# Kernel optimization log

Measured on AMD Instinct MI355X. Metric: run time of the kernel, lower is better.

## Reference

```python
import jax, jax.numpy as jnp
import numpy as np

B, S, D, NH, A, K, N_ITER = 512, 200, 512, 8, 512, 2, 3
DK = D // NH
L = 2 * K  # max local window length
NEG = -1e9


def make_pe_table(d, max_len):
    pos = np.arange(max_len)[:, None].astype(np.float64)
    j = np.arange(d)[None, :]
    ang = pos / np.power(10000.0, 2.0 * (j // 2) / d)
    pe = np.zeros((max_len, d))
    pe[:, 0::2] = np.sin(ang[:, 0::2])
    pe[:, 1::2] = np.cos(ang[:, 1::2])
    pe = np.concatenate([np.zeros((1, d)), pe], axis=0)  # pad row at index 0
    return jnp.asarray(pe, jnp.float32)


def layer_norm(x, g, b, eps=1e-5):
    m = jnp.mean(x, axis=-1, keepdims=True)
    v = jnp.mean((x - m) ** 2, axis=-1, keepdims=True)
    return (x - m) / jnp.sqrt(v + eps) * g + b


def setup_inputs() -> dict:
    key = jax.random.key(0)
    ks = jax.random.split(key, 24)
    p = lambda k, shape, s=0.02: jax.random.normal(k, shape, jnp.float32) * s
    embedded = jax.random.normal(ks[0], (B, S, D), jnp.float32)
    stc_lens = jax.random.randint(ks[1], (B,), 8, S + 1, jnp.int32)
    offsets = jnp.minimum(jax.random.randint(ks[2], (B,), 0, S, jnp.int32), stc_lens - 1)
    sep_lst = jnp.sort(jax.random.randint(ks[3], (B, 2), 0, S, jnp.int32), axis=1)
    return dict(
        embedded=embedded, stc_lens=stc_lens, offsets=offsets, sep_lst=sep_lst,
        W1=p(ks[4], (D, A)), W2=p(ks[5], (A, 1)),
        ln_g=jnp.ones((D,), jnp.float32), ln_b=jnp.zeros((D,), jnp.float32),
        lng_g=jnp.ones((D,), jnp.float32), lng_b=jnp.zeros((D,), jnp.float32),
        Wq=p(ks[6], (D, D)), bq=jnp.zeros((D,), jnp.float32),
        Wk=p(ks[7], (D, D)), bk=jnp.zeros((D,), jnp.float32),
        Wv=p(ks[8], (D, D)), bv=jnp.zeros((D,), jnp.float32),
        W_ih=p(ks[9], (3 * D, D)), W_hh=p(ks[10], (3 * D, D)),
        b_ih=jnp.zeros((3 * D,), jnp.float32), b_hh=jnp.zeros((3 * D,), jnp.float32),
        seg_emb=p(ks[11], (2, D)),
        pe_table=make_pe_table(D, S),
    )


def _forward(embedded, W1, W2, ln_g, ln_b, lng_g, lng_b, Wq, bq, Wk, bk, Wv, bv,
             W_ih, W_hh, b_ih, b_hh, seg_emb, pe_table, stc_lens, offsets, sep_lst):
    nsep = sep_lst.shape[1]
    bidx = jnp.arange(B)
    # ---- LocalVisiblePooling: per-sample window [start, end) around offset ----
    idx = jnp.sum(sep_lst < offsets[:, None], axis=1)  # segment index containing pos
    prev_sep = sep_lst[bidx, jnp.clip(idx - 1, 0, nsep - 1)]
    left = jnp.where(idx > 0, prev_sep + 1, 0)
    next_sep = sep_lst[bidx, jnp.clip(idx, 0, nsep - 1)]
    right = jnp.where(idx < nsep, next_sep, stc_lens)
    start = jnp.maximum(offsets - K, left)
    end = jnp.minimum(offsets + K, right)
    inds = start[:, None] + jnp.arange(L)  # [B, L]
    valid = inds < end[:, None]
    ic = jnp.clip(inds, 0, S - 1)
    h_blk = embedded[bidx[:, None], ic] * valid[..., None].astype(embedded.dtype)  # [B,L,D]
    a = jnp.tanh(h_blk @ W1) @ W2  # [B, L, 1]
    s1 = jax.nn.softmax(a[..., 0], axis=0)  # faithful to Softmax(dim=1) over batch dim
    score = jax.nn.softmax(jnp.where(valid, s1, NEG), axis=1)  # masked softmax over window
    b0_bf = jnp.einsum('bl,bld->bd', score, h_blk)  # [B, D]
    # ---- relative positional encoding for H ----
    x = jnp.arange(S)[None, :]  # [1, S]
    pos = offsets[:, None]
    ip = jnp.where(x < pos, pos - x, x + 1 - pos)
    ip = jnp.where(x < stc_lens[:, None], ip, 0)
    ip = jnp.clip(ip, 0, S)
    seg = (x >= pos).astype(jnp.int32)
    H = embedded + pe_table[ip] + seg_emb[seg]  # [B, S, D]
    H = layer_norm(H, ln_g, ln_b)
    b_t = layer_norm(b0_bf + pe_table[0], ln_g, ln_b)  # 'b' pe is the zero pad row
    # ---- GlobalUpdate: sigmoid-attention MHA (q_len=1) + GRUCell, N iterations ----
    pad = x >= stc_lens[:, None]  # [B, S] True where padded
    kproj = (H @ Wk + bk).reshape(B, S, NH, DK)
    vproj = (H @ Wv + bv).reshape(B, S, NH, DK)
    scale = 1.0 / jnp.sqrt(jnp.float32(DK))
    for _ in range(N_ITER):
        q = (b_t @ Wq + bq).reshape(B, NH, DK)
        scores = jnp.einsum('bhd,bshd->bhs', q, kproj) * scale
        scores = jnp.where(pad[:, None, :], NEG, scores)
        p_attn = jax.nn.sigmoid(scores)  # non-standard sigmoid attention
        m_t = jnp.einsum('bhs,bshd->bhd', p_attn, vproj).reshape(B, D)
        m_t = layer_norm(m_t, lng_g, lng_b)
        gi = m_t @ W_ih.T + b_ih
        gh = b_t @ W_hh.T + b_hh
        ir, iz, inn = jnp.split(gi, 3, axis=-1)
        hr, hz, hn = jnp.split(gh, 3, axis=-1)
        r = jax.nn.sigmoid(ir + hr)
        z = jax.nn.sigmoid(iz + hz)
        n = jnp.tanh(inn + r * hn)
        b_t = (1.0 - z) * n + z * b_t
    return b_t[:, None, :]  # [B, 1, D]


def reference(embedded, stc_lens, offsets, sep_lst, W1, W2, ln_g, ln_b, lng_g, lng_b,
              Wq, bq, Wk, bk, Wv, bv, W_ih, W_hh, b_ih, b_hh, seg_emb, pe_table):
    return _forward(embedded, W1, W2, ln_g, ln_b, lng_g, lng_b, Wq, bq, Wk, bk, Wv, bv,
                    W_ih, W_hh, b_ih, b_hh, seg_emb, pe_table, stc_lens, offsets, sep_lst)
```

## Files before the change

### kernel.cpp

```cpp
#include <hip/hip_runtime.h>
#include <hip/hip_bf16.h>
#include <math.h>

constexpr int B_   = 512;
constexpr int S_   = 200;
constexpr int D_   = 512;
constexpr int NH_  = 8;
constexpr int DK_  = 64;
constexpr int LBLK = 4;
constexpr int NITER = 3;
constexpr int TD_  = 1536;
#define NEGV (-1000000000.0f)

using bf16 = __hip_bfloat16;
typedef __attribute__((ext_vector_type(8))) short bf16x8;
typedef __attribute__((ext_vector_type(4))) float f32x4;

__device__ __forceinline__ float wred(float x) {
#pragma unroll
    for (int o = 32; o; o >>= 1) x += __shfl_xor(x, o);
    return x;
}

__global__ void __launch_bounds__(256) k_cvt(const float* __restrict__ src,
                                             bf16* __restrict__ dst, int n) {
    int i = blockIdx.x * 256 + threadIdx.x;
    if (i < n) dst[i] = __float2bfloat16(src[i]);
}

__global__ void __launch_bounds__(256) k_tcvt(const float* __restrict__ src,
                                              bf16* __restrict__ dst) {
    int i = blockIdx.x * 256 + threadIdx.x;
    if (i >= D_ * TD_) return;
    int k = i / TD_, n = i - k * TD_;
    dst[i] = __float2bfloat16(src[n * D_ + k]);
}

__global__ void __launch_bounds__(256) k_blockscore(
        const float* __restrict__ emb, const float* __restrict__ W1,
        const float* __restrict__ W2, const int* __restrict__ stc,
        const int* __restrict__ offs, const int* __restrict__ sep,
        float* __restrict__ hblk, float* __restrict__ a_out,
        int* __restrict__ se_out) {
    int b = blockIdx.x;
    int t = threadIdx.x;
    int off = offs[b], slen = stc[b];
    int sA = sep[b * 2 + 0], sB = sep[b * 2 + 1];
    int idx = (sA < off ? 1 : 0) + (sB < off ? 1 : 0);
    int prev = (idx == 2) ? sB : sA;
    int nxt  = (idx == 0) ? sA : sB;
    int left = (idx > 0) ? prev + 1 : 0;
    int right = (idx < 2) ? nxt : slen;
    int start = max(off - 2, left);
    int end   = min(off + 2, right);

    __shared__ float hs[LBLK][D_];
    {
        int l = t >> 6, lane = t & 63;
        int ind = start + l;
        bool valid = ind < end;
        float v0x=0,v0y=0,v0z=0,v0w=0,v1x=0,v1y=0,v1z=0,v1w=0;
        if (valid) {
            int ic = min(max(ind, 0), S_ - 1);
            const float* src = emb + ((size_t)b * S_ + ic) * D_ + lane * 8;
            float4 u0 = *(const float4*)src;
            float4 u1 = *(const float4*)(src + 4);
            v0x=u0.x; v0y=u0.y; v0z=u0.z; v0w=u0.w;
            v1x=u1.x; v1y=u1.y; v1z=u1.z; v1w=u1.w;
        }
        int base = lane * 8;
        hs[l][base+0]=v0x; hs[l][base+1]=v0y; hs[l][base+2]=v0z; hs[l][base+3]=v0w;
        hs[l][base+4]=v1x; hs[l][base+5]=v1y; hs[l][base+6]=v1z; hs[l][base+7]=v1w;
        float* g = hblk + ((size_t)b * LBLK + l) * D_ + base;
        g[0]=v0x; g[1]=v0y; g[2]=v0z; g[3]=v0w; g[4]=v1x; g[5]=v1y; g[6]=v1z; g[7]=v1w;
    }
    __syncthreads();

    float pa0 = 0.f, pa1 = 0.f, pa2 = 0.f, pa3 = 0.f;
#pragma unroll
    for (int cc = 0; cc < 2; ++cc) {
        int col = t + cc * 256;
        float a0 = 0.f, a1 = 0.f, a2 = 0.f, a3 = 0.f;
        for (int d = 0; d < D_; ++d) {
            float w = W1[(size_t)d * 512 + col];
            a0 += hs[0][d] * w; a1 += hs[1][d] * w;
            a2 += hs[2][d] * w; a3 += hs[3][d] * w;
        }
        float w2 = W2[col];
        pa0 += tanhf(a0) * w2; pa1 += tanhf(a1) * w2;
        pa2 += tanhf(a2) * w2; pa3 += tanhf(a3) * w2;
    }
    __shared__ float red[256];
    float pv[4] = {pa0, pa1, pa2, pa3};
#pragma unroll
    for (int l = 0; l < 4; ++l) {
        red[t] = pv[l]; __syncthreads();
        for (int st = 128; st; st >>= 1) {
            if (t < st) red[t] += red[t + st];
            __syncthreads();
        }
        if (t == 0) a_out[b * 4 + l] = red[0];
        __syncthreads();
    }
    if (t == 0) { se_out[b * 2] = start; se_out[b * 2 + 1] = end; }
}

__global__ void __launch_bounds__(512) k_score(const float* __restrict__ a_in,
                                               const int* __restrict__ se,
                                               float* __restrict__ score) {
    int b = threadIdx.x;
    float av[4], s1[4];
#pragma unroll
    for (int l = 0; l < 4; ++l) av[l] = a_in[b * 4 + l];
    __shared__ float red[512];
#pragma unroll
    for (int l = 0; l < 4; ++l) {
        red[b] = av[l]; __syncthreads();
        for (int st = 256; st; st >>= 1) {
            if (b < st) red[b] = fmaxf(red[b], red[b + st]);
            __syncthreads();
        }
        float mx = red[0]; __syncthreads();
        float e = expf(av[l] - mx);
        red[b] = e; __syncthreads();
        for (int st = 256; st; st >>= 1) {
            if (b < st) red[b] += red[b + st];
            __syncthreads();
        }
        s1[l] = e / red[0];
        __syncthreads();
    }
    int start = se[b * 2], end = se[b * 2 + 1];
    float x[4], mx2 = -1e30f;
#pragma unroll
    for (int l = 0; l < 4; ++l) {
        x[l] = (start + l < end) ? s1[l] : NEGV;
        mx2 = fmaxf(mx2, x[l]);
    }
    float s = 0.f, e4[4];
#pragma unroll
    for (int l = 0; l < 4; ++l) { e4[l] = expf(x[l] - mx2); s += e4[l]; }
    float inv = 1.f / s;
#pragma unroll
    for (int l = 0; l < 4; ++l) score[b * 4 + l] = e4[l] * inv;
}

__global__ void __launch_bounds__(64) k_b0(
        const float* __restrict__ hblk, const float* __restrict__ score,
        const float* __restrict__ pe, const float* __restrict__ g,
        const float* __restrict__ bb, float* __restrict__ bt,
        bf16* __restrict__ btb) {
    int b = blockIdx.x, lane = threadIdx.x;
    float sc0 = score[b*4+0], sc1 = score[b*4+1], sc2 = score[b*4+2], sc3 = score[b*4+3];
    const float* hb = hblk + (size_t)b * LBLK * D_ + lane * 8;
    float v[8];
#pragma unroll
    for (int j = 0; j < 8; ++j) {
        float x = pe[lane * 8 + j];
        x += sc0 * hb[j] + sc1 * hb[D_ + j] + sc2 * hb[2*D_ + j] + sc3 * hb[3*D_ + j];
        v[j] = x;
    }
    float sum = 0.f;
#pragma unroll
    for (int j = 0; j < 8; ++j) sum += v[j];
    sum = wred(sum);
    float mean = sum * (1.f / 512.f);
    float sq = 0.f;
#pragma unroll
    for (int j = 0; j < 8; ++j) { float c = v[j] - mean; sq += c * c; }
    sq = wred(sq);
    float rstd = rsqrtf(sq * (1.f / 512.f) + 1e-5f);
#pragma unroll
    for (int j = 0; j < 8; ++j) {
        int d = lane * 8 + j;
        float y = (v[j] - mean) * rstd * g[d] + bb[d];
        bt[(size_t)b * D_ + d] = y;
        btb[(size_t)b * D_ + d] = __float2bfloat16(y);
    }
}

__global__ void __launch_bounds__(256) k_H(
        const float* __restrict__ emb, const float* __restrict__ pe,
        const float* __restrict__ seg_emb, const float* __restrict__ g,
        const float* __restrict__ bb, const int* __restrict__ stc,
        const int* __restrict__ offs, bf16* __restrict__ Hc,
        int b0, int nrows) {
    int rid = blockIdx.x * 4 + (threadIdx.x >> 6);
    if (rid >= nrows) return;
    int lane = threadIdx.x & 63;
    int bl = rid / S_;
    int s = rid - bl * S_;
    int b = b0 + bl;
    int slen = stc[b];
    if (s >= slen) return;
    int pos = offs[b];
    int ip = (s < pos) ? (pos - s) : (s + 1 - pos);
    if (ip > S_) ip = S_;
    int seg = (s >= pos) ? 1 : 0;
    const float* er = emb + ((size_t)b * S_ + s) * D_ + lane * 8;
    const float* pr = pe + (size_t)ip * D_ + lane * 8;
    const float* sr = seg_emb + seg * D_ + lane * 8;
    float4 e0 = *(const float4*)er, e1 = *(const float4*)(er + 4);
    float4 p0 = *(const float4*)pr, p1 = *(const float4*)(pr + 4);
    float4 q0 = *(const float4*)sr, q1 = *(const float4*)(sr + 4);
    float v[8];
    v[0]=e0.x+p0.x+q0.x; v[1]=e0.y+p0.y+q0.y; v[2]=e0.z+p0.z+q0.z; v[3]=e0.w+p0.w+q0.w;
    v[4]=e1.x+p1.x+q1.x; v[5]=e1.y+p1.y+q1.y; v[6]=e1.z+p1.z+q1.z; v[7]=e1.w+p1.w+q1.w;
    float sum = 0.f;
#pragma unroll
    for (int j = 0; j < 8; ++j) sum += v[j];
    sum = wred(sum);
    float mean = sum * (1.f / 512.f);
    float sq = 0.f;
#pragma unroll
    for (int j = 0; j < 8; ++j) { float c = v[j] - mean; sq += c * c; }
    sq = wred(sq);
    float rstd = rsqrtf(sq * (1.f / 512.f) + 1e-5f);
    union { uint4 u; bf16 h[8]; } o;
#pragma unroll
    for (int j = 0; j < 8; ++j) {
        int d = lane * 8 + j;
        o.h[j] = __float2bfloat16((v[j] - mean) * rstd * g[d] + bb[d]);
    }
    *(uint4*)(Hc + ((size_t)bl * S_ + s) * D_ + lane * 8) = o.u;
}

__device__ __forceinline__ void gemm_tile64(
        const bf16* __restrict__ Abase, int lda,
        const bf16* __restrict__ Bbase, int ldb,
        const float* __restrict__ bias,
        float* __restrict__ Cf, bf16* __restrict__ Cb, int ldc,
        int rows_valid) {
    __shared__ bf16 As[64][40];
    __shared__ bf16 BsT[64][40];
    int t = threadIdx.x;
    int lane = t & 63, w = t >> 6;
    f32x4 acc0 = {0.f,0.f,0.f,0.f}, acc1 = {0.f,0.f,0.f,0.f};
    f32x4 acc2 = {0.f,0.f,0.f,0.f}, acc3 = {0.f,0.f,0.f,0.f};
    int arow = t >> 2, ac8 = (t & 3) * 8;
    int bn = t & 63, bkb = (t >> 6) * 8;

    for (int k0 = 0; k0 < 512; k0 += 32) {
        *(uint4*)&As[arow][ac8] =
            *(const uint4*)(Abase + (size_t)arow * lda + k0 + ac8);
        {
            union { uint4 u; bf16 h[8]; } tmp;
#pragma unroll
            for (int j = 0; j < 8; ++j)
                tmp.h[j] = Bbase[(size_t)(k0 + bkb + j) * ldb + bn];
            *(uint4*)&BsT[bn][bkb] = tmp.u;
        }
        __syncthreads();
        bf16x8 bfrag = *(const bf16x8*)&BsT[w * 16 + (lane & 15)][(lane >> 4) * 8];
        bf16x8 a0 = *(const bf16x8*)&As[ 0 + (lane & 15)][(lane >> 4) * 8];
        bf16x8 a1 = *(const bf16x8*)&As[16 + (lane & 15)][(lane >> 4) * 8];
        bf16x8 a2 = *(const bf16x8*)&As[32 + (lane & 15)][(lane >> 4) * 8];
        bf16x8 a3 = *(const bf16x8*)&As[48 + (lane & 15)][(lane >> 4) * 8];
        acc0 = __builtin_amdgcn_mfma_f32_16x16x32_bf16(a0, bfrag, acc0, 0, 0, 0);
        acc1 = __builtin_amdgcn_mfma_f32_16x16x32_bf16(a1, bfrag, acc1, 0, 0, 0);
        acc2 = __builtin_amdgcn_mfma_f32_16x16x32_bf16(a2, bfrag, acc2, 0, 0, 0);
        acc3 = __builtin_amdgcn_mfma_f32_16x16x32_bf16(a3, bfrag, acc3, 0, 0, 0);
        __syncthreads();
    }
    int col = w * 16 + (lane & 15);
    float bvv = bias[col];
    int rbase = (lane >> 4) * 4;
    f32x4 av[4] = {acc0, acc1, acc2, acc3};
#pragma unroll
    for (int rb = 0; rb < 4; ++rb) {
#pragma unroll
        for (int r = 0; r < 4; ++r) {
            int row = rb * 16 + rbase + r;
            if (row < rows_valid) {
                float vv = av[rb][r] + bvv;
                if (Cf) Cf[(size_t)row * ldc + col] = vv;
                if (Cb) Cb[(size_t)row * ldc + col] = __float2bfloat16(vv);
            }
        }
    }
}

__global__ void __launch_bounds__(256) k_gemm_kv(
        const bf16* __restrict__ Hc, const bf16* __restrict__ Wk,
        const bf16* __restrict__ Wv, const float* __restrict__ bk,
        const float* __restrict__ bv, bf16* __restrict__ kvk,
        bf16* __restrict__ kvv, const int* __restrict__ stc, int b0) {
    int nt = blockIdx.x;
    int s0 = blockIdx.y * 64;
    int bl = blockIdx.z;
    int b = b0 + bl;
    int slen = stc[b];
    if (s0 >= slen) return;
    const bf16* A = Hc + ((size_t)bl * S_ + s0) * D_;
    const bf16* Bm; bf16* C; const float* bias; int n0;
    if (nt < 8) { Bm = Wk; C = kvk; bias = bk; n0 = nt * 64; }
    else        { Bm = Wv; C = kvv; bias = bv; n0 = (nt - 8) * 64; }
    int rows_valid = min(64, slen - s0);
    gemm_tile64(A, D_, Bm + n0, D_, bias + n0,
                nullptr, C + ((size_t)b * S_ + s0) * D_ + n0, D_, rows_valid);
}

__global__ void __launch_bounds__(256) k_gemm_flat(
        const bf16* __restrict__ A, int lda, const bf16* __restrict__ Bm, int ldb,
        const float* __restrict__ bias, float* __restrict__ Cf,
        bf16* __restrict__ Cb, int ldc) {
    int n0 = blockIdx.x * 64, m0 = blockIdx.y * 64;
    gemm_tile64(A + (size_t)m0 * lda, lda, Bm + n0, ldb, bias + n0,
                Cf ? Cf + (size_t)m0 * ldc + n0 : nullptr,
                Cb ? Cb + (size_t)m0 * ldc + n0 : nullptr, ldc, 64);
}

__global__ void __launch_bounds__(256) k_attn(
        const float* __restrict__ q, const bf16* __restrict__ kk,
        const bf16* __restrict__ vv, const int* __restrict__ stc,
        const float* __restrict__ lng_g, const float* __restrict__ lng_b,
        float* __restrict__ mf, bf16* __restrict__ mb) {
    int b = blockIdx.x;
    int t = threadIdx.x, w = t >> 6, lane = t & 63;
    int slen = stc[b];
    const float* qp = q + (size_t)b * D_ + lane * 8;
    float4 qa = *(const float4*)qp, qb4 = *(const float4*)(qp + 4);
    float qv[8] = {qa.x, qa.y, qa.z, qa.w, qb4.x, qb4.y, qb4.z, qb4.w};
    float acc[8] = {0,0,0,0,0,0,0,0};
    const bf16* kbase = kk + (size_t)b * S_ * D_ + lane * 8;
    const bf16* vbase = vv + (size_t)b * S_ * D_ + lane * 8;
    for (int s = w; s < slen; s += 4) {
        union { uint4 u; bf16 h[8]; } kl, vl;
        kl.u = *(const uint4*)(kbase + (size_t)s * D_);
        float part = 0.f;
#pragma unroll
        for (int j = 0; j < 8; ++j) part += qv[j] * __bfloat162float(kl.h[j]);
        part += __shfl_xor(part, 1);
        part += __shfl_xor(part, 2);
        part += __shfl_xor(part, 4);
        float p = 1.f / (1.f + __expf(-part * 0.125f));
        vl.u = *(const uint4*)(vbase + (size_t)s * D_);
#pragma unroll
        for (int j = 0; j < 8; ++j) acc[j] += p * __bfloat162float(vl.h[j]);
    }
    __shared__ float macc[4][D_];
#pragma unroll
    for (int j = 0; j < 8; ++j) macc[w][lane * 8 + j] = acc[j];
    __syncthreads();
    __shared__ float red[256];
    int d1 = t + 256;
    float x0 = macc[0][t] + macc[1][t] + macc[2][t] + macc[3][t];
    float x1 = macc[0][d1] + macc[1][d1] + macc[2][d1] + macc[3][d1];
    red[t] = x0 + x1; __syncthreads();
    for (int st = 128; st; st >>= 1) {
        if (t < st) red[t] += red[t + st];
        __syncthreads();
    }
    float mean = red[0] * (1.f / 512.f); __syncthreads();
    float c0 = x0 - mean, c1 = x1 - mean;
    red[t] = c0 * c0 + c1 * c1; __syncthreads();
    for (int st = 128; st; st >>= 1) {
        if (t < st) red[t] += red[t + st];
        __syncthreads();
    }
    float rstd = rsqrtf(red[0] * (1.f / 512.f) + 1e-5f);
    float y0 = c0 * rstd * lng_g[t] + lng_b[t];
    float y1 = c1 * rstd * lng_g[d1] + lng_b[d1];
    mf[(size_t)b * D_ + t] = y0;
    mf[(size_t)b * D_ + d1] = y1;
    mb[(size_t)b * D_ + t] = __float2bfloat16(y0);
    mb[(size_t)b * D_ + d1] = __float2bfloat16(y1);
}

__global__ void __launch_bounds__(256) k_gru(
        const float* __restrict__ gi, const float* __restrict__ gh,
        float* __restrict__ bt, bf16* __restrict__ btb) {
    int i = blockIdx.x * 256 + threadIdx.x;
    int b = i >> 9, d = i & 511;
    const float* gib = gi + (size_t)b * TD_;
    const float* ghb = gh + (size_t)b * TD_;
    float ir = gib[d], iz = gib[512 + d], inn = gib[1024 + d];
    float hr = ghb[d], hz = ghb[512 + d], hn = ghb[1024 + d];
    float r = 1.f / (1.f + expf(-(ir + hr)));
    float z = 1.f / (1.f + expf(-(iz + hz)));
    float n = tanhf(inn + r * hn);
    float bo = bt[i];
    float bn = (1.f - z) * n + z * bo;
    bt[i] = bn;
    btb[i] = __float2bfloat16(bn);
}

extern "C" void kernel_launch(void* const* d_in, const int* in_sizes, int n_in,
                              void* d_out, int out_size, void* d_ws, size_t ws_size,
                              hipStream_t stream) {
    const float* emb   = (const float*)d_in[0];
    const int*   stc   = (const int*)d_in[1];
    const int*   offs  = (const int*)d_in[2];
    const int*   sep   = (const int*)d_in[3];
    const float* W1    = (const float*)d_in[4];
    const float* W2    = (const float*)d_in[5];
    const float* ln_g  = (const float*)d_in[6];
    const float* ln_b  = (const float*)d_in[7];
    const float* lng_g = (const float*)d_in[8];
    const float* lng_b = (const float*)d_in[9];
    const float* Wq    = (const float*)d_in[10];
    const float* bq    = (const float*)d_in[11];
    const float* Wk    = (const float*)d_in[12];
    const float* bk    = (const float*)d_in[13];
    const float* Wv    = (const float*)d_in[14];
    const float* bv    = (const float*)d_in[15];
    const float* W_ih  = (const float*)d_in[16];
    const float* W_hh  = (const float*)d_in[17];
    const float* b_ih  = (const float*)d_in[18];
    const float* b_hh  = (const float*)d_in[19];
    const float* seg_e = (const float*)d_in[20];
    const float* pe    = (const float*)d_in[21];

    char* base = (char*)d_ws;
    size_t off = 0;
    auto alloc = [&](size_t bytes) -> void* {
        off = (off + 255) & ~(size_t)255;
        void* r = base + off;
        off += bytes;
        return r;
    };
    bf16* kvk = (bf16*)alloc((size_t)(B_ * S_ + 64) * D_ * 2);
    bf16* kvv = (bf16*)alloc((size_t)(B_ * S_ + 64) * D_ * 2);
    float* hblk = (float*)alloc((size_t)B_ * LBLK * D_ * 4);
    float* a_s  = (float*)alloc((size_t)B_ * 4 * 4);
    float* scr  = (float*)alloc((size_t)B_ * 4 * 4);
    int*   se   = (int*)alloc((size_t)B_ * 2 * 4);
    float* bt   = (float*)alloc((size_t)B_ * D_ * 4);
    bf16*  btb  = (bf16*)alloc((size_t)B_ * D_ * 2);
    float* qb   = (float*)alloc((size_t)B_ * D_ * 4);
    float* mf   = (float*)alloc((size_t)B_ * D_ * 4);
    bf16*  mb   = (bf16*)alloc((size_t)B_ * D_ * 2);
    float* gi   = (float*)alloc((size_t)B_ * TD_ * 4);
    float* gh   = (float*)alloc((size_t)B_ * TD_ * 4);
    bf16* Wq_b  = (bf16*)alloc((size_t)D_ * D_ * 2);
    bf16* Wk_b  = (bf16*)alloc((size_t)D_ * D_ * 2);
    bf16* Wv_b  = (bf16*)alloc((size_t)D_ * D_ * 2);
    bf16* WihT  = (bf16*)alloc((size_t)D_ * TD_ * 2);
    bf16* WhhT  = (bf16*)alloc((size_t)D_ * TD_ * 2);

    auto hbytes = [](int ch) { return ((size_t)ch * S_ + 64) * D_ * 2; };
    int CH = 512;
    {
        size_t used = (off + 255) & ~(size_t)255;
        size_t remain = (ws_size > used) ? (ws_size - used) : 0;
        if (hbytes(512) + 256 > remain) CH = 64;
        if (CH == 64 && hbytes(64) + 256 > remain) CH = 16;
    }
    bf16* Hc = (bf16*)alloc(hbytes(CH));

    k_cvt<<<(D_ * D_ + 255) / 256, 256, 0, stream>>>(Wq, Wq_b, D_ * D_);
    k_cvt<<<(D_ * D_ + 255) / 256, 256, 0, stream>>>(Wk, Wk_b, D_ * D_);
    k_cvt<<<(D_ * D_ + 255) / 256, 256, 0, stream>>>(Wv, Wv_b, D_ * D_);
    k_tcvt<<<(D_ * TD_ + 255) / 256, 256, 0, stream>>>(W_ih, WihT);
    k_tcvt<<<(D_ * TD_ + 255) / 256, 256, 0, stream>>>(W_hh, WhhT);

    k_blockscore<<<B_, 256, 0, stream>>>(emb, W1, W2, stc, offs, sep, hblk, a_s, se);
    k_score<<<1, 512, 0, stream>>>(a_s, se, scr);
    k_b0<<<B_, 64, 0, stream>>>(hblk, scr, pe, ln_g, ln_b, bt, btb);

    for (int c = 0; c < B_; c += CH) {
        int rows = CH * S_;
        k_H<<<(rows + 3) / 4, 256, 0, stream>>>(emb, pe, seg_e, ln_g, ln_b,
                                                stc, offs, Hc, c, rows);
        k_gemm_kv<<<dim3(16, 4, CH), 256, 0, stream>>>(Hc, Wk_b, Wv_b, bk, bv,
                                                       kvk, kvv, stc, c);
    }

    for (int it = 0; it < NITER; ++it) {
        k_gemm_flat<<<dim3(8, 8), 256, 0, stream>>>(btb, D_, Wq_b, D_, bq,
                                                    qb, nullptr, D_);
        k_attn<<<B_, 256, 0, stream>>>(qb, kvk, kvv, stc, lng_g, lng_b, mf, mb);
        k_gemm_flat<<<dim3(24, 8), 256, 0, stream>>>(mb, D_, WihT, TD_, b_ih,
                                                     gi, nullptr, TD_);
        k_gemm_flat<<<dim3(24, 8), 256, 0, stream>>>(btb, D_, WhhT, TD_, b_hh,
                                                     gh, nullptr, TD_);
        k_gru<<<(B_ * D_) / 256, 256, 0, stream>>>(gi, gh, bt, btb);
    }
    hipMemcpyAsync(d_out, bt, (size_t)out_size * sizeof(float),
                   hipMemcpyDeviceToDevice, stream);
}
```

Before: 844.2 us.

## Rework GEMMs with N-major weights, LDS direct loads, fused K/V and gate launches

Weights are pre-transposed to N-by-K bf16 layout so both GEMM operands can be loaded into LDS with direct global-to-LDS 16-byte loads, replacing the strided scalar B gathers. A templated GEMM core supports larger tiles, and K and V projections are fused into one 64x256-tiled GEMM writing an interleaved KV buffer. The two GRU gate GEMMs now share one launch, and the weight conversions are merged into a single prep kernel. The interleaved KV layout changes attention's memory stride, and the larger tiles reduce the number of blocks.

```diff
diff --git a/kernel.cpp b/kernel.cpp
--- a/kernel.cpp
+++ b/kernel.cpp
@@ -5,8 +5,6 @@
 constexpr int B_   = 512;
 constexpr int S_   = 200;
 constexpr int D_   = 512;
-constexpr int NH_  = 8;
-constexpr int DK_  = 64;
 constexpr int LBLK = 4;
 constexpr int NITER = 3;
 constexpr int TD_  = 1536;
@@ -22,18 +20,38 @@
     return x;
 }
 
-__global__ void __launch_bounds__(256) k_cvt(const float* __restrict__ src,
-                                             bf16* __restrict__ dst, int n) {
+__device__ __forceinline__ void gload16(const bf16* g, bf16* l) {
+    __builtin_amdgcn_global_load_lds(
+        (const __attribute__((address_space(1))) void*)g,
+        (__attribute__((address_space(3))) void*)l, 16, 0, 0);
+}
+
+__global__ void __launch_bounds__(256) k_prep(
+        const float* __restrict__ Wq, const float* __restrict__ Wk,
+        const float* __restrict__ Wv, const float* __restrict__ bk,
+        const float* __restrict__ bv, const float* __restrict__ Wih,
+        const float* __restrict__ Whh, bf16* __restrict__ WqT,
+        bf16* __restrict__ WkvT, float* __restrict__ bkv,
+        bf16* __restrict__ Wih_b, bf16* __restrict__ Whh_b) {
     int i = blockIdx.x * 256 + threadIdx.x;
-    if (i < n) dst[i] = __float2bfloat16(src[i]);
-}
-
-__global__ void __launch_bounds__(256) k_tcvt(const float* __restrict__ src,
-                                              bf16* __restrict__ dst) {
-    int i = blockIdx.x * 256 + threadIdx.x;
-    if (i >= D_ * TD_) return;
-    int k = i / TD_, n = i - k * TD_;
-    dst[i] = __float2bfloat16(src[n * D_ + k]);
+    if (i < 512 * 512) {
+        int n = i >> 9, k = i & 511;
+        WqT[i] = __float2bfloat16(Wq[k * 512 + n]);
+        return;
+    }
+    i -= 512 * 512;
+    if (i < 1024 * 512) {
+        int n = i >> 9, k = i & 511;
+        WkvT[i] = __float2bfloat16(n < 512 ? Wk[k * 512 + n]
+                                           : Wv[k * 512 + (n - 512)]);
+        return;
+    }
+    i -= 1024 * 512;
+    if (i < TD_ * D_) { Wih_b[i] = __float2bfloat16(Wih[i]); return; }
+    i -= TD_ * D_;
+    if (i < TD_ * D_) { Whh_b[i] = __float2bfloat16(Whh[i]); return; }
+    i -= TD_ * D_;
+    if (i < 1024) bkv[i] = (i < 512) ? bk[i] : bv[i - 512];
 }
 
 __global__ void __launch_bounds__(256) k_blockscore(
@@ -225,96 +243,129 @@
     *(uint4*)(Hc + ((size_t)bl * S_ + s) * D_ + lane * 8) = o.u;
 }
 
-__device__ __forceinline__ void gemm_tile64(
-        const bf16* __restrict__ Abase, int lda,
-        const bf16* __restrict__ Bbase, int ldb,
+template<int BM, int BN, int NWM, int NWN, bool OUT_BF16>
+__device__ __forceinline__ void gemm_core(
+        const bf16* __restrict__ A, int lda,
+        const bf16* __restrict__ Bnk, int ldb,
         const float* __restrict__ bias,
-        float* __restrict__ Cf, bf16* __restrict__ Cb, int ldc,
-        int rows_valid) {
-    __shared__ bf16 As[64][40];
-    __shared__ bf16 BsT[64][40];
-    int t = threadIdx.x;
-    int lane = t & 63, w = t >> 6;
-    f32x4 acc0 = {0.f,0.f,0.f,0.f}, acc1 = {0.f,0.f,0.f,0.f};
-    f32x4 acc2 = {0.f,0.f,0.f,0.f}, acc3 = {0.f,0.f,0.f,0.f};
-    int arow = t >> 2, ac8 = (t & 3) * 8;
-    int bn = t & 63, bkb = (t >> 6) * 8;
+        void* __restrict__ Cout, int ldc, int rows_valid) {
+    constexpr int NW = NWM * NWN;
+    constexpr int FM = BM / (NWM * 16);
+    constexpr int FN = BN / (NWN * 16);
+    constexpr int IA = BM / (16 * NW);
+    constexpr int IB = BN / (16 * NW);
+    __shared__ bf16 As[BM * 32];
+    __shared__ bf16 Bs[BN * 32];
+    int t = threadIdx.x, lane = t & 63, w = t >> 6;
+    int wm = w / NWN, wn = w % NWN;
+    int sr = lane >> 2;
+    int sc = (lane & 3) * 8;
+
+    f32x4 acc[FM][FN];
+#pragma unroll
+    for (int i = 0; i < FM; ++i)
+#pragma unroll
+        for (int j = 0; j < FN; ++j) acc[i][j] = f32x4{0.f,0.f,0.f,0.f};
 
     for (int k0 = 0; k0 < 512; k0 += 32) {
-        *(uint4*)&As[arow][ac8] =
-            *(const uint4*)(Abase + (size_t)arow * lda + k0 + ac8);
-        {
-            union { uint4 u; bf16 h[8]; } tmp;
-#pragma unroll
-            for (int j = 0; j < 8; ++j)
-                tmp.h[j] = Bbase[(size_t)(k0 + bkb + j) * ldb + bn];
-            *(uint4*)&BsT[bn][bkb] = tmp.u;
+#pragma unroll
+        for (int j = 0; j < IA; ++j) {
+            int r = (w * IA + j) * 16 + sr;
+            gload16(A + (size_t)r * lda + k0 + sc, &As[(w * IA + j) * 512]);
+        }
+#pragma unroll
+        for (int j = 0; j < IB; ++j) {
+            int r = (w * IB + j) * 16 + sr;
+            gload16(Bnk + (size_t)r * ldb + k0 + sc, &Bs[(w * IB + j) * 512]);
         }
         __syncthreads();
-        bf16x8 bfrag = *(const bf16x8*)&BsT[w * 16 + (lane & 15)][(lane >> 4) * 8];
-        bf16x8 a0 = *(const bf16x8*)&As[ 0 + (lane & 15)][(lane >> 4) * 8];
-        bf16x8 a1 = *(const bf16x8*)&As[16 + (lane & 15)][(lane >> 4) * 8];
-        bf16x8 a2 = *(const bf16x8*)&As[32 + (lane & 15)][(lane >> 4) * 8];
-        bf16x8 a3 = *(const bf16x8*)&As[48 + (lane & 15)][(lane >> 4) * 8];
-        acc0 = __builtin_amdgcn_mfma_f32_16x16x32_bf16(a0, bfrag, acc0, 0, 0, 0);
-        acc1 = __builtin_amdgcn_mfma_f32_16x16x32_bf16(a1, bfrag, acc1, 0, 0, 0);
-        acc2 = __builtin_amdgcn_mfma_f32_16x16x32_bf16(a2, bfrag, acc2, 0, 0, 0);
-        acc3 = __builtin_amdgcn_mfma_f32_16x16x32_bf16(a3, bfrag, acc3, 0, 0, 0);
+        bf16x8 af[FM], bfr[FN];
+#pragma unroll
+        for (int i = 0; i < FM; ++i)
+            af[i] = *(const bf16x8*)&As[((wm * FM + i) * 16 + (lane & 15)) * 32
+                                        + (lane >> 4) * 8];
+#pragma unroll
+        for (int j = 0; j < FN; ++j)
+            bfr[j] = *(const bf16x8*)&Bs[((wn * FN + j) * 16 + (lane & 15)) * 32
+                                         + (lane >> 4) * 8];
+#pragma unroll
+        for (int i = 0; i < FM; ++i)
+#pragma unroll
+            for (int j = 0; j < FN; ++j)
+                acc[i][j] = __builtin_amdgcn_mfma_f32_16x16x32_bf16(
+                                af[i], bfr[j], acc[i][j], 0, 0, 0);
         __syncthreads();
     }
-    int col = w * 16 + (lane & 15);
-    float bvv = bias[col];
-    int rbase = (lane >> 4) * 4;
-    f32x4 av[4] = {acc0, acc1, acc2, acc3};
-#pragma unroll
-    for (int rb = 0; rb < 4; ++rb) {
-#pragma unroll
-        for (int r = 0; r < 4; ++r) {
-            int row = rb * 16 + rbase + r;
-            if (row < rows_valid) {
-                float vv = av[rb][r] + bvv;
-                if (Cf) Cf[(size_t)row * ldc + col] = vv;
-                if (Cb) Cb[(size_t)row * ldc + col] = __float2bfloat16(vv);
+    int coln = wn * FN * 16 + (lane & 15);
+    int rowb = (lane >> 4) * 4;
+#pragma unroll
+    for (int j = 0; j < FN; ++j) {
+        int col = coln + j * 16;
+        float bvv = bias[col];
+#pragma unroll
+        for (int i = 0; i < FM; ++i) {
+            int rbase = (wm * FM + i) * 16 + rowb;
+#pragma unroll
+            for (int rr = 0; rr < 4; ++rr) {
+                int row = rbase + rr;
+                if (row < rows_valid) {
+                    float v = acc[i][j][rr] + bvv;
+                    if (OUT_BF16)
+                        ((bf16*)Cout)[(size_t)row * ldc + col] = __float2bfloat16(v);
+                    else
+                        ((float*)Cout)[(size_t)row * ldc + col] = v;
+                }
             }
         }
     }
 }
 
-__global__ void __launch_bounds__(256) k_gemm_kv(
-        const bf16* __restrict__ Hc, const bf16* __restrict__ Wk,
-        const bf16* __restrict__ Wv, const float* __restrict__ bk,
-        const float* __restrict__ bv, bf16* __restrict__ kvk,
-        bf16* __restrict__ kvv, const int* __restrict__ stc, int b0) {
-    int nt = blockIdx.x;
-    int s0 = blockIdx.y * 64;
+__global__ void __launch_bounds__(256) k_gemm_kv2(
+        const bf16* __restrict__ Hc, const bf16* __restrict__ WkvT,
+        const float* __restrict__ bkv, bf16* __restrict__ kv,
+        const int* __restrict__ stc, int b0) {
     int bl = blockIdx.z;
     int b = b0 + bl;
+    int s0 = blockIdx.y * 64;
     int slen = stc[b];
     if (s0 >= slen) return;
-    const bf16* A = Hc + ((size_t)bl * S_ + s0) * D_;
-    const bf16* Bm; bf16* C; const float* bias; int n0;
-    if (nt < 8) { Bm = Wk; C = kvk; bias = bk; n0 = nt * 64; }
-    else        { Bm = Wv; C = kvv; bias = bv; n0 = (nt - 8) * 64; }
-    int rows_valid = min(64, slen - s0);
-    gemm_tile64(A, D_, Bm + n0, D_, bias + n0,
-                nullptr, C + ((size_t)b * S_ + s0) * D_ + n0, D_, rows_valid);
-}
-
-__global__ void __launch_bounds__(256) k_gemm_flat(
-        const bf16* __restrict__ A, int lda, const bf16* __restrict__ Bm, int ldb,
-        const float* __restrict__ bias, float* __restrict__ Cf,
-        bf16* __restrict__ Cb, int ldc) {
+    int n0 = blockIdx.x * 256;
+    gemm_core<64, 256, 1, 4, true>(
+        Hc + ((size_t)bl * S_ + s0) * D_, D_,
+        WkvT + (size_t)n0 * 512, 512, bkv + n0,
+        kv + ((size_t)b * S_ + s0) * 1024 + n0, 1024,
+        min(64, slen - s0));
+}
+
+__global__ void __launch_bounds__(256) k_gemm_q(
+        const bf16* __restrict__ btb, const bf16* __restrict__ WqT,
+        const float* __restrict__ bq, float* __restrict__ qb) {
     int n0 = blockIdx.x * 64, m0 = blockIdx.y * 64;
-    gemm_tile64(A + (size_t)m0 * lda, lda, Bm + n0, ldb, bias + n0,
-                Cf ? Cf + (size_t)m0 * ldc + n0 : nullptr,
-                Cb ? Cb + (size_t)m0 * ldc + n0 : nullptr, ldc, 64);
+    gemm_core<64, 64, 2, 2, false>(
+        btb + (size_t)m0 * D_, D_, WqT + (size_t)n0 * 512, 512, bq + n0,
+        qb + (size_t)m0 * D_ + n0, D_, 64);
+}
+
+__global__ void __launch_bounds__(256) k_gemm_gates(
+        const bf16* __restrict__ mb, const bf16* __restrict__ btb,
+        const bf16* __restrict__ Wih_b, const bf16* __restrict__ Whh_b,
+        const float* __restrict__ b_ih, const float* __restrict__ b_hh,
+        float* __restrict__ gi, float* __restrict__ gh) {
+    int n0 = blockIdx.x * 128, m0 = blockIdx.y * 64;
+    const bf16* A  = blockIdx.z ? btb : mb;
+    const bf16* Bm = blockIdx.z ? Whh_b : Wih_b;
+    const float* bias = blockIdx.z ? b_hh : b_ih;
+    float* C = blockIdx.z ? gh : gi;
+    gemm_core<64, 128, 2, 2, false>(
+        A + (size_t)m0 * D_, D_, Bm + (size_t)n0 * 512, 512, bias + n0,
+        C + (size_t)m0 * TD_ + n0, TD_, 64);
 }
 
 __global__ void __launch_bounds__(256) k_attn(
-        const float* __restrict__ q, const bf16* __restrict__ kk,
-        const bf16* __restrict__ vv, const int* __restrict__ stc,
-        const float* __restrict__ lng_g, const float* __restrict__ lng_b,
-        float* __restrict__ mf, bf16* __restrict__ mb) {
+        const float* __restrict__ q, const bf16* __restrict__ kv,
+        const int* __restrict__ stc, const float* __restrict__ lng_g,
+        const float* __restrict__ lng_b, float* __restrict__ mf,
+        bf16* __restrict__ mb) {
     int b = blockIdx.x;
     int t = threadIdx.x, w = t >> 6, lane = t & 63;
     int slen = stc[b];
@@ -322,11 +373,10 @@
     float4 qa = *(const float4*)qp, qb4 = *(const float4*)(qp + 4);
     float qv[8] = {qa.x, qa.y, qa.z, qa.w, qb4.x, qb4.y, qb4.z, qb4.w};
     float acc[8] = {0,0,0,0,0,0,0,0};
-    const bf16* kbase = kk + (size_t)b * S_ * D_ + lane * 8;
-    const bf16* vbase = vv + (size_t)b * S_ * D_ + lane * 8;
+    const bf16* kvb = kv + (size_t)b * S_ * 1024 + lane * 8;
     for (int s = w; s < slen; s += 4) {
         union { uint4 u; bf16 h[8]; } kl, vl;
-        kl.u = *(const uint4*)(kbase + (size_t)s * D_);
+        kl.u = *(const uint4*)(kvb + (size_t)s * 1024);
         float part = 0.f;
 #pragma unroll
         for (int j = 0; j < 8; ++j) part += qv[j] * __bfloat162float(kl.h[j]);
@@ -334,7 +384,7 @@
         part += __shfl_xor(part, 2);
         part += __shfl_xor(part, 4);
         float p = 1.f / (1.f + __expf(-part * 0.125f));
-        vl.u = *(const uint4*)(vbase + (size_t)s * D_);
+        vl.u = *(const uint4*)(kvb + (size_t)s * 1024 + 512);
 #pragma unroll
         for (int j = 0; j < 8; ++j) acc[j] += p * __bfloat162float(vl.h[j]);
     }
@@ -419,8 +469,7 @@
         off += bytes;
         return r;
     };
-    bf16* kvk = (bf16*)alloc((size_t)(B_ * S_ + 64) * D_ * 2);
-    bf16* kvv = (bf16*)alloc((size_t)(B_ * S_ + 64) * D_ * 2);
+    bf16* kv   = (bf16*)alloc(((size_t)B_ * S_ + 64) * 1024 * 2);
     float* hblk = (float*)alloc((size_t)B_ * LBLK * D_ * 4);
     float* a_s  = (float*)alloc((size_t)B_ * 4 * 4);
     float* scr  = (float*)alloc((size_t)B_ * 4 * 4);
@@ -432,11 +481,11 @@
     bf16*  mb   = (bf16*)alloc((size_t)B_ * D_ * 2);
     float* gi   = (float*)alloc((size_t)B_ * TD_ * 4);
     float* gh   = (float*)alloc((size_t)B_ * TD_ * 4);
-    bf16* Wq_b  = (bf16*)alloc((size_t)D_ * D_ * 2);
-    bf16* Wk_b  = (bf16*)alloc((size_t)D_ * D_ * 2);
-    bf16* Wv_b  = (bf16*)alloc((size_t)D_ * D_ * 2);
-    bf16* WihT  = (bf16*)alloc((size_t)D_ * TD_ * 2);
-    bf16* WhhT  = (bf16*)alloc((size_t)D_ * TD_ * 2);
+    bf16* WqT   = (bf16*)alloc((size_t)D_ * D_ * 2);
+    bf16* WkvT  = (bf16*)alloc((size_t)1024 * 512 * 2);
+    float* bkv  = (float*)alloc((size_t)1024 * 4);
+    bf16* Wih_b = (bf16*)alloc((size_t)TD_ * D_ * 2);
+    bf16* Whh_b = (bf16*)alloc((size_t)TD_ * D_ * 2);
 
     auto hbytes = [](int ch) { return ((size_t)ch * S_ + 64) * D_ * 2; };
     int CH = 512;
@@ -448,11 +497,11 @@
     }
     bf16* Hc = (bf16*)alloc(hbytes(CH));
 
-    k_cvt<<<(D_ * D_ + 255) / 256, 256, 0, stream>>>(Wq, Wq_b, D_ * D_);
-    k_cvt<<<(D_ * D_ + 255) / 256, 256, 0, stream>>>(Wk, Wk_b, D_ * D_);
-    k_cvt<<<(D_ * D_ + 255) / 256, 256, 0, stream>>>(Wv, Wv_b, D_ * D_);
-    k_tcvt<<<(D_ * TD_ + 255) / 256, 256, 0, stream>>>(W_ih, WihT);
-    k_tcvt<<<(D_ * TD_ + 255) / 256, 256, 0, stream>>>(W_hh, WhhT);
+    {
+        int total = 512*512 + 1024*512 + 2*TD_*D_ + 1024;
+        k_prep<<<(total + 255) / 256, 256, 0, stream>>>(
+            Wq, Wk, Wv, bk, bv, W_ih, W_hh, WqT, WkvT, bkv, Wih_b, Whh_b);
+    }
 
     k_blockscore<<<B_, 256, 0, stream>>>(emb, W1, W2, stc, offs, sep, hblk, a_s, se);
     k_score<<<1, 512, 0, stream>>>(a_s, se, scr);
@@ -462,18 +511,14 @@
         int rows = CH * S_;
         k_H<<<(rows + 3) / 4, 256, 0, stream>>>(emb, pe, seg_e, ln_g, ln_b,
                                                 stc, offs, Hc, c, rows);
-        k_gemm_kv<<<dim3(16, 4, CH), 256, 0, stream>>>(Hc, Wk_b, Wv_b, bk, bv,
-                                                       kvk, kvv, stc, c);
+        k_gemm_kv2<<<dim3(4, 4, CH), 256, 0, stream>>>(Hc, WkvT, bkv, kv, stc, c);
     }
 
     for (int it = 0; it < NITER; ++it) {
-        k_gemm_flat<<<dim3(8, 8), 256, 0, stream>>>(btb, D_, Wq_b, D_, bq,
-                                                    qb, nullptr, D_);
-        k_attn<<<B_, 256, 0, stream>>>(qb, kvk, kvv, stc, lng_g, lng_b, mf, mb);
-        k_gemm_flat<<<dim3(24, 8), 256, 0, stream>>>(mb, D_, WihT, TD_, b_ih,
-                                                     gi, nullptr, TD_);
-        k_gemm_flat<<<dim3(24, 8), 256, 0, stream>>>(btb, D_, WhhT, TD_, b_hh,
-                                                     gh, nullptr, TD_);
+        k_gemm_q<<<dim3(8, 8), 256, 0, stream>>>(btb, WqT, bq, qb);
+        k_attn<<<B_, 256, 0, stream>>>(qb, kv, stc, lng_g, lng_b, mf, mb);
+        k_gemm_gates<<<dim3(12, 8, 2), 256, 0, stream>>>(mb, btb, Wih_b, Whh_b,
+                                                         b_ih, b_hh, gi, gh);
         k_gru<<<(B_ * D_) / 256, 256, 0, stream>>>(gi, gh, bt, btb);
     }
     hipMemcpyAsync(d_out, bt, (size_t)out_size * sizeof(float),
```

After: 783.2 us. -7.2%, faster.
